# Kernel tuning notes

Measured on AMD Instinct MI355X. Metric: run time of the kernel, lower is better.

## Reference

```python
import jax, jax.numpy as jnp
import numpy as np

B, N = 16384, 4096
PERCENT_ON = 0.1
TEMPERATURE = 10.0  # training-mode temperature
K = int(round(N * PERCENT_ON))  # 410


def setup_inputs() -> dict:
    key = jax.random.key(0)
    k1, k2 = jax.random.split(key)
    x = jax.random.normal(k1, (B, N), dtype=jnp.float32)
    # Gumbel noise for sampling-without-replacement (Gumbel-top-k trick),
    # equivalent to torch.multinomial(softmax(x/T), k, replacement=False).
    gumbel = jax.random.gumbel(k2, (B, N), dtype=jnp.float32)
    return {"x": x, "gumbel": gumbel}


def reference(x, gumbel):
    # logits with temperature
    logits = x / TEMPERATURE
    # entropy of the categorical distribution per row, averaged (single stable pass)
    logp = jax.nn.log_softmax(logits, axis=-1)
    entropy = jnp.mean(-jnp.sum(jnp.exp(logp) * logp, axis=-1))
    # sample K winners without replacement via Gumbel-top-k
    _, idx = jax.lax.top_k(logits + gumbel, K)  # idx: [B, K]
    rows = jnp.arange(x.shape[0])[:, None]       # [B, 1]
    mask = jnp.zeros_like(x).at[rows, idx].set(1.0)
    out = x * mask  # relu=False path
    return out, entropy
```

## Files before the change

kernel.cpp:

```cpp
#include <hip/hip_runtime.h>
#include <math.h>

#define TPB 256
#define EPT 16
#define NN  4096
#define KSEL 410
#define CAP 1024

typedef float floatx4 __attribute__((ext_vector_type(4)));

__device__ __forceinline__ void dma16(const float* gsrc, float* lds) {
    __builtin_amdgcn_global_load_lds(
        (__attribute__((address_space(1))) void*)(void*)gsrc,
        (__attribute__((address_space(3))) void*)(void*)lds,
        16, 0, 0);
}

template <bool USE_WS>
__global__ __launch_bounds__(TPB)
void skw_main(const float* __restrict__ x, const float* __restrict__ g,
              float* __restrict__ out, float* __restrict__ rowH,
              float* __restrict__ entAcc, float invB)
{
    const int row  = blockIdx.x;
    const int t    = threadIdx.x;
    const int w    = t >> 6;
    const int lane = t & 63;
    const size_t rbase = (size_t)row * NN;

    unsigned bp[EPT / 4];

    __shared__ float    stage[2 * NN];
    __shared__ unsigned hist0[256][5];
    __shared__ unsigned wtot[4];
    __shared__ unsigned wtA[4], wtB[4];
    __shared__ float    fred[8];
    __shared__ unsigned sh_digit, sh_above, sh_cnt, sh_take, sh_eq;
    __shared__ float    sh_thr;

    float*   list = reinterpret_cast<float*>(&hist0[0][0]);
    floatx4* sx4  = reinterpret_cast<floatx4*>(stage);
    floatx4* ss4  = reinterpret_cast<floatx4*>(stage + NN);

    const float* xr = x + rbase;
    const float* gr = g + rbase;
    floatx4*     op = reinterpret_cast<floatx4*>(out + rbase);

#pragma unroll
    for (int q = 0; q < 4; ++q) {
        const int c = (q << 2) + w;
        dma16(xr + (c << 8) + (lane << 2), &stage[c << 8]);
        dma16(gr + (c << 8) + (lane << 2), &stage[NN + (c << 8)]);
    }

    unsigned* h0 = &hist0[0][0];
#pragma unroll
    for (int i = 0; i < 5; ++i) h0[t + 256 * i] = 0;
    if (t == 0) sh_cnt = 0;

    asm volatile("s_waitcnt vmcnt(0)" ::: "memory");

    float sZ = 0.f, sZL = 0.f;
#pragma unroll
    for (int q = 0; q < EPT / 4; ++q) {
        floatx4 xx = sx4[(q << 8) + t];
        floatx4 gg = ss4[(q << 8) + t];
        floatx4 so;
        unsigned pk = 0;
#pragma unroll
        for (int jj = 0; jj < 4; ++jj) {
            float xs = xx[jj];
            float l = xs * 0.1f;
            float e = __expf(l);
            sZ  += e;
            sZL = __builtin_fmaf(e, l, sZL);
            float q10 = __builtin_fmaf(__builtin_fmaf(-10.0f, l, xs), 0.1f, l);
            float s = q10 + gg[jj];
            so[jj] = s;
            int b = (int)__builtin_fmaf(s, 16.0f, 64.0f);
            b = min(max(b, 0), 255);
            pk |= (unsigned)b << (8 * jj);
        }
        ss4[(q << 8) + t] = so;
        bp[q] = pk;
    }

#pragma unroll
    for (int sft = 32; sft >= 1; sft >>= 1) { sZ += __shfl_xor(sZ, sft); sZL += __shfl_xor(sZL, sft); }
    if (lane == 0) { fred[w] = sZ; fred[4 + w] = sZL; }
    __syncthreads();

    if (t == 0) {
        float Z = fred[0] + fred[1] + fred[2] + fred[3];
        float L = fred[4] + fred[5] + fred[6] + fred[7];
        float H = __logf(Z) - L / Z;
        if (USE_WS) rowH[row] = H;
        else atomicAdd(entAcc, H * invB);
    }

#pragma unroll
    for (int q = 0; q < EPT / 4; ++q) {
        unsigned pk = bp[q];
#pragma unroll
        for (int jj = 0; jj < 4; ++jj)
            atomicAdd(&hist0[(pk >> (8 * jj)) & 255u][lane & 3], 1u);
    }
    __syncthreads();

    unsigned v = hist0[t][0] + hist0[t][1] + hist0[t][2] + hist0[t][3];
#pragma unroll
    for (int sft = 1; sft < 64; sft <<= 1) {
        unsigned tmp = __shfl(v, lane + sft);
        v += (lane + sft < 64) ? tmp : 0u;
    }
    if (lane == 0) wtot[w] = v;
    unsigned vnext = __shfl(v, lane + 1);
    __syncthreads();
    unsigned Kr = KSEL;
    {
        unsigned hi = 0;
#pragma unroll
        for (int c = 0; c < 4; ++c) hi += (c > w) ? wtot[c] : 0u;
        unsigned cum     = v + hi;
        unsigned cumNext = ((lane < 63) ? vnext : 0u) + hi;
        if (cum >= Kr && cumNext < Kr) { sh_digit = (unsigned)t; sh_above = cumNext; }
    }
    __syncthreads();
    const unsigned Bstar = sh_digit;
    Kr -= sh_above;

#pragma unroll
    for (int q = 0; q < EPT / 4; ++q) {
        unsigned pk = bp[q];
#pragma unroll
        for (int jj = 0; jj < 4; ++jj) {
            if (((pk >> (8 * jj)) & 255u) == Bstar) {
                unsigned p = atomicAdd(&sh_cnt, 1u);
                if (p < CAP) list[p] = stage[NN + (q << 10) + 4 * t + jj];
            }
        }
    }
    __syncthreads();

    const unsigned M = sh_cnt;
    for (unsigned i = t; i < M; i += TPB) {
        float ki = list[i];
        unsigned gt = 0, eqc = 0;
        for (unsigned j2 = 0; j2 < M; ++j2) {
            float kj = list[j2];
            gt  += (kj > ki)  ? 1u : 0u;
            eqc += (kj == ki) ? 1u : 0u;
        }
        if (gt < Kr && Kr <= gt + eqc) { sh_thr = ki; sh_take = Kr - gt; sh_eq = eqc; }
    }
    __syncthreads();
    const float    thr    = sh_thr;
    const unsigned KrTake = sh_take;
    const unsigned EqTot  = sh_eq;

    if (KrTake == EqTot) {
#pragma unroll
        for (int q = 0; q < EPT / 4; ++q) {
            floatx4 sq = ss4[(q << 8) + t];
            floatx4 xq = sx4[(q << 8) + t];
            floatx4 o4;
#pragma unroll
            for (int jj = 0; jj < 4; ++jj)
                o4[jj] = (sq[jj] >= thr) ? xq[jj] : 0.0f;
            __builtin_nontemporal_store(o4, &op[(q << 8) + t]);
        }
    } else {
        unsigned eq[4];
#pragma unroll
        for (int q = 0; q < 4; ++q) {
            floatx4 sq = ss4[(q << 8) + t];
            unsigned e = 0;
#pragma unroll
            for (int jj = 0; jj < 4; ++jj) e += (sq[jj] == thr) ? 1u : 0u;
            eq[q] = e;
        }
        unsigned wA = eq[0] | (eq[1] << 16);
        unsigned wB = eq[2] | (eq[3] << 16);
        unsigned sA = wA, sB = wB;
#pragma unroll
        for (int sft = 1; sft < 64; sft <<= 1) {
            unsigned ta = __shfl(sA, lane - sft);
            unsigned tb = __shfl(sB, lane - sft);
            if (lane >= sft) { sA += ta; sB += tb; }
        }
        if (lane == 63) { wtA[w] = sA; wtB[w] = sB; }
        __syncthreads();
        unsigned offA = 0, offB = 0, totA = 0, totB = 0;
#pragma unroll
        for (int c = 0; c < 4; ++c) {
            totA += wtA[c]; totB += wtB[c];
            if (c < w) { offA += wtA[c]; offB += wtB[c]; }
        }
        unsigned exA = offA + sA - wA;
        unsigned exB = offB + sB - wB;
        unsigned tot0 = totA & 0xFFFFu, tot1 = totA >> 16, tot2 = totB & 0xFFFFu;
        unsigned baseq[4] = {0u, tot0, tot0 + tot1, tot0 + tot1 + tot2};
        unsigned exq[4]   = {exA & 0xFFFFu, exA >> 16, exB & 0xFFFFu, exB >> 16};

#pragma unroll
        for (int q = 0; q < EPT / 4; ++q) {
            unsigned pos = baseq[q] + exq[q];
            floatx4 sq = ss4[(q << 8) + t];
            floatx4 xq = sx4[(q << 8) + t];
            floatx4 o4;
#pragma unroll
            for (int jj = 0; jj < 4; ++jj) {
                bool sel;
                if (sq[jj] > thr)        sel = true;
                else if (sq[jj] == thr)  { sel = (pos < KrTake); ++pos; }
                else                     sel = false;
                o4[jj] = sel ? xq[jj] : 0.0f;
            }
            __builtin_nontemporal_store(o4, &op[(q << 8) + t]);
        }
    }
}

__global__ void skw_zero(float* p) { *p = 0.0f; }

__global__ void skw_reduce(const float* __restrict__ rowH, float* __restrict__ outp, int B)
{
    __shared__ float red[256];
    int t = threadIdx.x;
    float s = 0.f;
    for (int i = t; i < B; i += 256) s += rowH[i];
    red[t] = s; __syncthreads();
    for (int st = 128; st > 0; st >>= 1) { if (t < st) red[t] += red[t + st]; __syncthreads(); }
    if (t == 0) *outp = red[0] / (float)B;
}

extern "C" void kernel_launch(void* const* d_in, const int* in_sizes, int n_in,
                              void* d_out, int out_size, void* d_ws, size_t ws_size,
                              hipStream_t stream)
{
    const float* x = (const float*)d_in[0];
    const float* g = (const float*)d_in[1];
    float* out = (float*)d_out;
    const int BN = in_sizes[0];
    const int B  = BN / NN;
    float* entp = out + (size_t)BN;

    if (ws_size >= (size_t)B * sizeof(float)) {
        float* rowH = (float*)d_ws;
        skw_main<true><<<B, TPB, 0, stream>>>(x, g, out, rowH, nullptr, 0.f);
        skw_reduce<<<1, 256, 0, stream>>>(rowH, entp, B);
    } else {
        skw_zero<<<1, 1, 0, stream>>>(entp);
        skw_main<false><<<B, TPB, 0, stream>>>(x, g, out, nullptr, entp, 1.0f / (float)B);
    }
}
```

Measured before the change: 163.3 us.

## Halve LDS staging by holding x in registers and reusing buffer for gumbel

The x row is DMA'd into LDS, copied into per-thread registers, and the same LDS buffer is then refilled with the gumbel row. The entropy sums are computed while the gumbel load is in flight. Cutting LDS per block roughly in half, together with launch bounds asking for 8 blocks, is meant to raise occupancy and hide memory latency. The cost is the gumbel load now runs after the x load instead of alongside it, plus extra registers to hold x.

```diff
diff --git a/kernel.cpp b/kernel.cpp
--- a/kernel.cpp
+++ b/kernel.cpp
@@ -17,7 +17,7 @@
 }
 
 template <bool USE_WS>
-__global__ __launch_bounds__(TPB)
+__global__ __launch_bounds__(TPB, 8)
 void skw_main(const float* __restrict__ x, const float* __restrict__ g,
               float* __restrict__ out, float* __restrict__ rowH,
               float* __restrict__ entAcc, float invB)
@@ -28,9 +28,10 @@
     const int lane = t & 63;
     const size_t rbase = (size_t)row * NN;
 
+    float    xv[EPT];
     unsigned bp[EPT / 4];
 
-    __shared__ float    stage[2 * NN];
+    __shared__ float    stage[NN];
     __shared__ unsigned hist0[256][5];
     __shared__ unsigned wtot[4];
     __shared__ unsigned wtA[4], wtB[4];
@@ -39,8 +40,7 @@
     __shared__ float    sh_thr;
 
     float*   list = reinterpret_cast<float*>(&hist0[0][0]);
-    floatx4* sx4  = reinterpret_cast<floatx4*>(stage);
-    floatx4* ss4  = reinterpret_cast<floatx4*>(stage + NN);
+    floatx4* ss4  = reinterpret_cast<floatx4*>(stage);
 
     const float* xr = x + rbase;
     const float* gr = g + rbase;
@@ -50,7 +50,6 @@
     for (int q = 0; q < 4; ++q) {
         const int c = (q << 2) + w;
         dma16(xr + (c << 8) + (lane << 2), &stage[c << 8]);
-        dma16(gr + (c << 8) + (lane << 2), &stage[NN + (c << 8)]);
     }
 
     unsigned* h0 = &hist0[0][0];
@@ -59,21 +58,46 @@
     if (t == 0) sh_cnt = 0;
 
     asm volatile("s_waitcnt vmcnt(0)" ::: "memory");
+    __builtin_amdgcn_sched_barrier(0);
+
+#pragma unroll
+    for (int q = 0; q < EPT / 4; ++q) {
+        floatx4 xq = ss4[(q << 8) + t];
+#pragma unroll
+        for (int jj = 0; jj < 4; ++jj) xv[4 * q + jj] = xq[jj];
+    }
+    asm volatile("s_waitcnt lgkmcnt(0)" ::: "memory");
+
+#pragma unroll
+    for (int q = 0; q < 4; ++q) {
+        const int c = (q << 2) + w;
+        dma16(gr + (c << 8) + (lane << 2), &stage[c << 8]);
+    }
 
     float sZ = 0.f, sZL = 0.f;
 #pragma unroll
-    for (int q = 0; q < EPT / 4; ++q) {
-        floatx4 xx = sx4[(q << 8) + t];
+    for (int j = 0; j < EPT; ++j) {
+        float l = xv[j] * 0.1f;
+        float e = __expf(l);
+        sZ  += e;
+        sZL = __builtin_fmaf(e, l, sZL);
+    }
+#pragma unroll
+    for (int sft = 32; sft >= 1; sft >>= 1) { sZ += __shfl_xor(sZ, sft); sZL += __shfl_xor(sZL, sft); }
+    if (lane == 0) { fred[w] = sZ; fred[4 + w] = sZL; }
+
+    asm volatile("s_waitcnt vmcnt(0)" ::: "memory");
+    __builtin_amdgcn_sched_barrier(0);
+
+#pragma unroll
+    for (int q = 0; q < EPT / 4; ++q) {
         floatx4 gg = ss4[(q << 8) + t];
         floatx4 so;
         unsigned pk = 0;
 #pragma unroll
         for (int jj = 0; jj < 4; ++jj) {
-            float xs = xx[jj];
-            float l = xs * 0.1f;
-            float e = __expf(l);
-            sZ  += e;
-            sZL = __builtin_fmaf(e, l, sZL);
+            float xs = xv[4 * q + jj];
+            float l  = xs * 0.1f;
             float q10 = __builtin_fmaf(__builtin_fmaf(-10.0f, l, xs), 0.1f, l);
             float s = q10 + gg[jj];
             so[jj] = s;
@@ -84,10 +108,6 @@
         ss4[(q << 8) + t] = so;
         bp[q] = pk;
     }
-
-#pragma unroll
-    for (int sft = 32; sft >= 1; sft >>= 1) { sZ += __shfl_xor(sZ, sft); sZL += __shfl_xor(sZL, sft); }
-    if (lane == 0) { fred[w] = sZ; fred[4 + w] = sZL; }
     __syncthreads();
 
     if (t == 0) {
@@ -136,7 +156,7 @@
         for (int jj = 0; jj < 4; ++jj) {
             if (((pk >> (8 * jj)) & 255u) == Bstar) {
                 unsigned p = atomicAdd(&sh_cnt, 1u);
-                if (p < CAP) list[p] = stage[NN + (q << 10) + 4 * t + jj];
+                if (p < CAP) list[p] = stage[(q << 10) + 4 * t + jj];
             }
         }
     }
@@ -162,11 +182,10 @@
 #pragma unroll
         for (int q = 0; q < EPT / 4; ++q) {
             floatx4 sq = ss4[(q << 8) + t];
-            floatx4 xq = sx4[(q << 8) + t];
             floatx4 o4;
 #pragma unroll
             for (int jj = 0; jj < 4; ++jj)
-                o4[jj] = (sq[jj] >= thr) ? xq[jj] : 0.0f;
+                o4[jj] = (sq[jj] >= thr) ? xv[4 * q + jj] : 0.0f;
             __builtin_nontemporal_store(o4, &op[(q << 8) + t]);
         }
     } else {
@@ -206,7 +225,6 @@
         for (int q = 0; q < EPT / 4; ++q) {
             unsigned pos = baseq[q] + exq[q];
             floatx4 sq = ss4[(q << 8) + t];
-            floatx4 xq = sx4[(q << 8) + t];
             floatx4 o4;
 #pragma unroll
             for (int jj = 0; jj < 4; ++jj) {
@@ -214,7 +232,7 @@
                 if (sq[jj] > thr)        sel = true;
                 else if (sq[jj] == thr)  { sel = (pos < KrTake); ++pos; }
                 else                     sel = false;
-                o4[jj] = sel ? xq[jj] : 0.0f;
+                o4[jj] = sel ? xv[4 * q + jj] : 0.0f;
             }
             __builtin_nontemporal_store(o4, &op[(q << 8) + t]);
         }
```

After: 164.0 us. No clear change (+0.4%).
